# Optimization experiments

Hardware: AMD Instinct MI355X
Metric: run time of the kernel (lower is better)

Reference implementation:

```python
import jax, jax.numpy as jnp
import numpy as np

B, S, H, NH = 2, 2048, 1024, 16
HD = H // NH  # 64


def rope_cos_sin(seq_len, dim, base=10000.0, dtype=jnp.float32):
    inv_freq = 1.0 / (base ** (jnp.arange(0, dim, 2, dtype=jnp.float32) / dim))
    t = jnp.arange(seq_len, dtype=jnp.float32)
    freqs = jnp.outer(t, inv_freq)              # [S, dim/2]
    emb = jnp.concatenate([freqs, freqs], -1)   # [S, dim]
    # broadcast shape [1, S, 1, dim]
    return jnp.cos(emb)[None, :, None, :].astype(dtype), jnp.sin(emb)[None, :, None, :].astype(dtype)


def rotate_half(x):
    x1, x2 = x[..., : x.shape[-1] // 2], x[..., x.shape[-1] // 2:]
    return jnp.concatenate([-x2, x1], axis=-1)


def setup_inputs() -> dict:
    key = jax.random.key(0)
    ks = jax.random.split(key, 5)
    sc = 1.0 / np.sqrt(H)
    x = jax.random.normal(ks[0], (B, S, H), jnp.float32)
    Wq = jax.random.normal(ks[1], (H, H), jnp.float32) * sc
    Wk = jax.random.normal(ks[2], (H, H), jnp.float32) * sc
    Wv = jax.random.normal(ks[3], (H, H), jnp.float32) * sc
    Wo = jax.random.normal(ks[4], (H, H), jnp.float32) * sc
    z = jnp.zeros((H,), jnp.float32)
    mask = jnp.tril(jnp.ones((S, S), bool))[None, None]  # causal [1,1,S,S]
    return {"x": x, "Wq": Wq, "bq": z, "Wk": Wk, "bk": z, "Wv": Wv, "bv": z,
            "Wo": Wo, "bo": z, "mask": mask}


def reference(x, Wq, bq, Wk, bk, Wv, bv, Wo, bo, mask):
    b, s, _ = x.shape
    q = (x @ Wq.T + bq).reshape(b, s, NH, HD)
    k = (x @ Wk.T + bk).reshape(b, s, NH, HD)
    v = (x @ Wv.T + bv).reshape(b, s, NH, HD)
    cos, sin = rope_cos_sin(s, HD, dtype=x.dtype)
    q = q * cos + rotate_half(q) * sin
    k = k * cos + rotate_half(k) * sin
    # [b, h, s, s] scores, explicit as in original
    scores = jnp.einsum("bqhd,bkhd->bhqk", q, k) / jnp.sqrt(jnp.asarray(HD, x.dtype))
    scores = jnp.where(mask, scores, jnp.asarray(-jnp.inf, x.dtype))
    attn = jax.nn.softmax(scores, axis=-1)
    out = jnp.einsum("bhqk,bkhd->bqhd", attn, v).reshape(b, s, H)
    return out @ Wo.T + bo
```

## Files before the change

### kernel.cpp

```cpp
#include <hip/hip_runtime.h>

typedef __bf16 bf16;
typedef __bf16 bf16x4 __attribute__((ext_vector_type(4)));
typedef __bf16 bf16x8 __attribute__((ext_vector_type(8)));
typedef float floatx4 __attribute__((ext_vector_type(4)));

#define MFMA16(a, b, c) __builtin_amdgcn_mfma_f32_16x16x32_bf16(a, b, c, 0, 0, 0)

__device__ __forceinline__ void load_lds16(const void* g, void* l) {
    __builtin_amdgcn_global_load_lds(
        (const __attribute__((address_space(1))) unsigned int*)g,
        (__attribute__((address_space(3))) unsigned int*)l, 16, 0, 0);
}

__device__ __forceinline__ bf16x8 scale8(bf16x8 a, float s) {
    bf16x8 o;
    #pragma unroll
    for (int i = 0; i < 8; i++) o[i] = (bf16)((float)a[i] * s);
    return o;
}

__global__ __launch_bounds__(256) void cvt_all_kernel(
    const float* __restrict__ x, const float* __restrict__ wq,
    const float* __restrict__ wk, const float* __restrict__ wv,
    const float* __restrict__ wo,
    bf16* __restrict__ xb, bf16* __restrict__ wqb, bf16* __restrict__ wkb,
    bf16* __restrict__ wvb, bf16* __restrict__ wob)
{
    int bid = blockIdx.x;
    const float* src; bf16* dst; int off;
    if (bid < 4096)      { src = x;  dst = xb;  off = bid; }
    else if (bid < 5120) { src = wq; dst = wqb; off = bid - 4096; }
    else if (bid < 6144) { src = wk; dst = wkb; off = bid - 5120; }
    else if (bid < 7168) { src = wv; dst = wvb; off = bid - 6144; }
    else                 { src = wo; dst = wob; off = bid - 7168; }
    int idx = (off * 256 + threadIdx.x) * 4;
    float4 v = *(const float4*)&src[idx];
    bf16x4 o;
    o[0] = (bf16)v.x; o[1] = (bf16)v.y; o[2] = (bf16)v.z; o[3] = (bf16)v.w;
    *(bf16x4*)&dst[idx] = o;
}

__global__ __launch_bounds__(256) void cvt_kernel(const float* __restrict__ x,
                                                  bf16* __restrict__ xb) {
    int idx = (blockIdx.x * 256 + threadIdx.x) * 4;
    float4 v = *(const float4*)&x[idx];
    bf16x4 o;
    o[0] = (bf16)v.x; o[1] = (bf16)v.y; o[2] = (bf16)v.z; o[3] = (bf16)v.w;
    *(bf16x4*)&xb[idx] = o;
}


#define PREP_STAGE()                                                          \
    int u0 = w * 128 + lane;                                                  \
    int u1 = u0 + 64;                                                         \
    int r0_ = u0 >> 2, c0_ = ((u0 & 3) ^ ((r0_ >> 1) & 3)) * 8;               \
    int r1_ = u1 >> 2, c1_ = ((u1 & 3) ^ ((r1_ >> 1) & 3)) * 8;               \
    int du0 = w * 1024;                                                       \
    int du1 = du0 + 512;

#define STAGE_PF(Asrc, Bsrc, arow, brow, sbuf, kk0)                           \
    do {                                                                      \
        load_lds16(&Asrc[(size_t)((arow) + r0_) * 1024 + (kk0) + c0_],        \
                   &As[sbuf][0][0] + du0);                                    \
        load_lds16(&Asrc[(size_t)((arow) + r1_) * 1024 + (kk0) + c1_],        \
                   &As[sbuf][0][0] + du1);                                    \
        load_lds16(&Bsrc[(size_t)((brow) + r0_) * 1024 + (kk0) + c0_],        \
                   &Bs[sbuf][0][0] + du0);                                    \
        load_lds16(&Bsrc[(size_t)((brow) + r1_) * 1024 + (kk0) + c1_],        \
                   &Bs[sbuf][0][0] + du1);                                    \
    } while (0)

#define GEMM_CORE(Asrc, Bsrc, arow, brow)                                     \
    PREP_STAGE()                                                              \
    STAGE_PF(Asrc, Bsrc, arow, brow, 0, 0);                                   \
    _Pragma("unroll 2")                                                       \
    for (int s = 0; s < 32; s++) {                                            \
        int sb = s & 1;                                                       \
        __syncthreads();                                                      \
        if (s + 1 < 32) STAGE_PF(Asrc, Bsrc, arow, brow, sb ^ 1, (s + 1) * 32); \
        bf16x8 af[4], bfr[4];                                                 \
        _Pragma("unroll")                                                     \
        for (int mt = 0; mt < 4; mt++) {                                      \
            int row = wm + mt * 16 + l15;                                     \
            af[mt] = *(const bf16x8*)&As[sb][row][(quad ^ ((row >> 1) & 3)) * 8]; \
        }                                                                     \
        _Pragma("unroll")                                                     \
        for (int nt = 0; nt < 4; nt++) {                                      \
            int row = wn + nt * 16 + l15;                                     \
            bfr[nt] = *(const bf16x8*)&Bs[sb][row][(quad ^ ((row >> 1) & 3)) * 8]; \
        }                                                                     \
        _Pragma("unroll")                                                     \
        for (int mt = 0; mt < 4; mt++)                                        \
            _Pragma("unroll")                                                 \
            for (int nt = 0; nt < 4; nt++)                                    \
                acc[mt][nt] = MFMA16(af[mt], bfr[nt], acc[mt][nt]);           \
    }

__global__ __launch_bounds__(256) void gemm_qkv_fast(
    const bf16* __restrict__ xb,
    const bf16* __restrict__ Wq, const bf16* __restrict__ Wk,
    const bf16* __restrict__ Wv,
    const float* __restrict__ bq, const float* __restrict__ bk,
    const float* __restrict__ bv,
    bf16* __restrict__ q_ws, bf16* __restrict__ k_ws, bf16* __restrict__ vt_ws)
{
    int m0 = blockIdx.x * 128;
    int n0 = blockIdx.y * 128;
    int sec = n0 >> 10;
    int nw0 = n0 & 1023;
    const bf16* W     = (sec == 0) ? Wq : (sec == 1) ? Wk : Wv;
    const float* bias = (sec == 0) ? bq : (sec == 1) ? bk : bv;

    __shared__ bf16 As[2][128][32];
    __shared__ bf16 Bs[2][128][32];

    int tid = threadIdx.x;
    int lane = tid & 63, w = tid >> 6;
    int l15 = lane & 15, quad = lane >> 4;
    int wm = (w >> 1) * 64, wn = (w & 1) * 64;

    floatx4 acc[4][4];
    #pragma unroll
    for (int i = 0; i < 4; i++)
        #pragma unroll
        for (int j = 0; j < 4; j++) acc[i][j] = (floatx4){0.f, 0.f, 0.f, 0.f};

    GEMM_CORE(xb, W, m0, nw0)

    if (sec < 2) {
        bf16* outp = (sec == 0) ? q_ws : k_ws;
        float inv[2];
        inv[0] = __expf(-(float)l15 * (9.210340371976184f / 32.0f));
        inv[1] = __expf(-(float)(16 + l15) * (9.210340371976184f / 32.0f));
        #pragma unroll
        for (int mt = 0; mt < 4; mt++) {
            #pragma unroll
            for (int r = 0; r < 4; r++) {
                int m = m0 + wm + mt * 16 + quad * 4 + r;
                int bb = m >> 11, s = m & 2047;
                #pragma unroll
                for (int nt = 0; nt < 2; nt++) {
                    int nl1 = nw0 + wn + nt * 16 + l15;
                    int nl2 = nl1 + 32;
                    float x1 = acc[mt][nt][r] + bias[nl1];
                    float x2 = acc[mt][nt + 2][r] + bias[nl2];
                    float ang = (float)s * inv[nt];
                    float sn, cs;
                    __sincosf(ang, &sn, &cs);
                    int hh = nl1 >> 6, d = nl1 & 63;
                    size_t base = ((size_t)(bb * 16 + hh) * 2048 + s) * 64;
                    outp[base + d]      = (bf16)(x1 * cs - x2 * sn);
                    outp[base + d + 32] = (bf16)(x2 * cs + x1 * sn);
                }
            }
        }
    } else {
        #pragma unroll
        for (int mt = 0; mt < 4; mt++) {
            int mbase = m0 + wm + mt * 16 + quad * 4;
            int bb = mbase >> 11, s0 = mbase & 2047;
            #pragma unroll
            for (int nt = 0; nt < 4; nt++) {
                int nl = nw0 + wn + nt * 16 + l15;
                int hh = nl >> 6, d = nl & 63;
                bf16x4 pk;
                #pragma unroll
                for (int r = 0; r < 4; r++) pk[r] = (bf16)(acc[mt][nt][r] + bias[nl]);
                *(bf16x4*)&vt_ws[((size_t)(bb * 16 + hh) * 64 + d) * 2048 + s0] = pk;
            }
        }
    }
}

__global__ __launch_bounds__(256) void gemm_out_fast(
    const bf16* __restrict__ A, const bf16* __restrict__ W,
    const float* __restrict__ bias, float* __restrict__ out)
{
    int m0 = blockIdx.x * 128;
    int n0 = blockIdx.y * 128;

    __shared__ bf16 As[2][128][32];
    __shared__ bf16 Bs[2][128][32];

    int tid = threadIdx.x;
    int lane = tid & 63, w = tid >> 6;
    int l15 = lane & 15, quad = lane >> 4;
    int wm = (w >> 1) * 64, wn = (w & 1) * 64;

    floatx4 acc[4][4];
    #pragma unroll
    for (int i = 0; i < 4; i++)
        #pragma unroll
        for (int j = 0; j < 4; j++) acc[i][j] = (floatx4){0.f, 0.f, 0.f, 0.f};

    GEMM_CORE(A, W, m0, n0)

    #pragma unroll
    for (int mt = 0; mt < 4; mt++) {
        #pragma unroll
        for (int r = 0; r < 4; r++) {
            int m = m0 + wm + mt * 16 + quad * 4 + r;
            #pragma unroll
            for (int nt = 0; nt < 4; nt++) {
                int nl = n0 + wn + nt * 16 + l15;
                out[(size_t)m * 1024 + nl] = acc[mt][nt][r] + bias[nl];
            }
        }
    }
}

__global__ __launch_bounds__(256) void gemm_qkv_f32w(
    const bf16* __restrict__ xb,
    const float* __restrict__ Wq, const float* __restrict__ Wk,
    const float* __restrict__ Wv,
    const float* __restrict__ bq, const float* __restrict__ bk,
    const float* __restrict__ bv,
    bf16* __restrict__ q_ws, bf16* __restrict__ k_ws, bf16* __restrict__ vt_ws)
{
    int m0 = blockIdx.x * 128;
    int n0 = blockIdx.y * 128;
    int sec = n0 >> 10;
    int nw0 = n0 & 1023;
    const float* W    = (sec == 0) ? Wq : (sec == 1) ? Wk : Wv;
    const float* bias = (sec == 0) ? bq : (sec == 1) ? bk : bv;

    __shared__ bf16 As[128][72];
    __shared__ bf16 Bs[128][72];

    int tid = threadIdx.x;
    int lane = tid & 63, w = tid >> 6;
    int l15 = lane & 15, quad = lane >> 4;
    int wm = (w >> 1) * 64, wn = (w & 1) * 64;
    int sr = tid >> 1;
    int sk = (tid & 1) * 32;

    floatx4 acc[4][4];
    #pragma unroll
    for (int i = 0; i < 4; i++)
        #pragma unroll
        for (int j = 0; j < 4; j++) acc[i][j] = (floatx4){0.f, 0.f, 0.f, 0.f};

    for (int k0 = 0; k0 < 1024; k0 += 64) {
        __syncthreads();
        const bf16* ap = &xb[(size_t)(m0 + sr) * 1024 + k0 + sk];
        bf16x8 a0 = *(const bf16x8*)(ap);
        bf16x8 a1 = *(const bf16x8*)(ap + 8);
        bf16x8 a2 = *(const bf16x8*)(ap + 16);
        bf16x8 a3 = *(const bf16x8*)(ap + 24);
        const float* wp = &W[(size_t)(nw0 + sr) * 1024 + k0 + sk];
        bf16x8 bv_[4];
        #pragma unroll
        for (int c = 0; c < 4; c++) {
            float4 f0 = *(const float4*)(wp + c * 8);
            float4 f1 = *(const float4*)(wp + c * 8 + 4);
            bf16x8 t;
            t[0] = (bf16)f0.x; t[1] = (bf16)f0.y; t[2] = (bf16)f0.z; t[3] = (bf16)f0.w;
            t[4] = (bf16)f1.x; t[5] = (bf16)f1.y; t[6] = (bf16)f1.z; t[7] = (bf16)f1.w;
            bv_[c] = t;
        }
        *(bf16x8*)&As[sr][sk + 0]  = a0;
        *(bf16x8*)&As[sr][sk + 8]  = a1;
        *(bf16x8*)&As[sr][sk + 16] = a2;
        *(bf16x8*)&As[sr][sk + 24] = a3;
        #pragma unroll
        for (int c = 0; c < 4; c++) *(bf16x8*)&Bs[sr][sk + c * 8] = bv_[c];
        __syncthreads();
        #pragma unroll
        for (int kk = 0; kk < 64; kk += 32) {
            bf16x8 af[4], bfr[4];
            #pragma unroll
            for (int mt = 0; mt < 4; mt++)
                af[mt] = *(const bf16x8*)&As[wm + mt * 16 + l15][kk + quad * 8];
            #pragma unroll
            for (int nt = 0; nt < 4; nt++)
                bfr[nt] = *(const bf16x8*)&Bs[wn + nt * 16 + l15][kk + quad * 8];
            #pragma unroll
            for (int mt = 0; mt < 4; mt++)
                #pragma unroll
                for (int nt = 0; nt < 4; nt++)
                    acc[mt][nt] = MFMA16(af[mt], bfr[nt], acc[mt][nt]);
        }
    }

    if (sec < 2) {
        bf16* outp = (sec == 0) ? q_ws : k_ws;
        float inv[2];
        inv[0] = __expf(-(float)l15 * (9.210340371976184f / 32.0f));
        inv[1] = __expf(-(float)(16 + l15) * (9.210340371976184f / 32.0f));
        #pragma unroll
        for (int mt = 0; mt < 4; mt++) {
            #pragma unroll
            for (int r = 0; r < 4; r++) {
                int m = m0 + wm + mt * 16 + quad * 4 + r;
                int bb = m >> 11, s = m & 2047;
                #pragma unroll
                for (int nt = 0; nt < 2; nt++) {
                    int nl1 = nw0 + wn + nt * 16 + l15;
                    int nl2 = nl1 + 32;
                    float x1 = acc[mt][nt][r] + bias[nl1];
                    float x2 = acc[mt][nt + 2][r] + bias[nl2];
                    float ang = (float)s * inv[nt];
                    float sn, cs;
                    __sincosf(ang, &sn, &cs);
                    int hh = nl1 >> 6, d = nl1 & 63;
                    size_t base = ((size_t)(bb * 16 + hh) * 2048 + s) * 64;
                    outp[base + d]      = (bf16)(x1 * cs - x2 * sn);
                    outp[base + d + 32] = (bf16)(x2 * cs + x1 * sn);
                }
            }
        }
    } else {
        #pragma unroll
        for (int mt = 0; mt < 4; mt++) {
            int mbase = m0 + wm + mt * 16 + quad * 4;
            int bb = mbase >> 11, s0 = mbase & 2047;
            #pragma unroll
            for (int nt = 0; nt < 4; nt++) {
                int nl = nw0 + wn + nt * 16 + l15;
                int hh = nl >> 6, d = nl & 63;
                bf16x4 pk;
                #pragma unroll
                for (int r = 0; r < 4; r++) pk[r] = (bf16)(acc[mt][nt][r] + bias[nl]);
                *(bf16x4*)&vt_ws[((size_t)(bb * 16 + hh) * 64 + d) * 2048 + s0] = pk;
            }
        }
    }
}

__global__ __launch_bounds__(256) void gemm_out_f32w(
    const bf16* __restrict__ A, const float* __restrict__ W,
    const float* __restrict__ bias, float* __restrict__ out)
{
    int m0 = blockIdx.x * 128;
    int n0 = blockIdx.y * 128;

    __shared__ bf16 As[128][72];
    __shared__ bf16 Bs[128][72];

    int tid = threadIdx.x;
    int lane = tid & 63, w = tid >> 6;
    int l15 = lane & 15, quad = lane >> 4;
    int wm = (w >> 1) * 64, wn = (w & 1) * 64;
    int sr = tid >> 1;
    int sk = (tid & 1) * 32;

    floatx4 acc[4][4];
    #pragma unroll
    for (int i = 0; i < 4; i++)
        #pragma unroll
        for (int j = 0; j < 4; j++) acc[i][j] = (floatx4){0.f, 0.f, 0.f, 0.f};

    for (int k0 = 0; k0 < 1024; k0 += 64) {
        __syncthreads();
        const bf16* ap = &A[(size_t)(m0 + sr) * 1024 + k0 + sk];
        bf16x8 a0 = *(const bf16x8*)(ap);
        bf16x8 a1 = *(const bf16x8*)(ap + 8);
        bf16x8 a2 = *(const bf16x8*)(ap + 16);
        bf16x8 a3 = *(const bf16x8*)(ap + 24);
        const float* wp = &W[(size_t)(n0 + sr) * 1024 + k0 + sk];
        bf16x8 bv_[4];
        #pragma unroll
        for (int c = 0; c < 4; c++) {
            float4 f0 = *(const float4*)(wp + c * 8);
            float4 f1 = *(const float4*)(wp + c * 8 + 4);
            bf16x8 t;
            t[0] = (bf16)f0.x; t[1] = (bf16)f0.y; t[2] = (bf16)f0.z; t[3] = (bf16)f0.w;
            t[4] = (bf16)f1.x; t[5] = (bf16)f1.y; t[6] = (bf16)f1.z; t[7] = (bf16)f1.w;
            bv_[c] = t;
        }
        *(bf16x8*)&As[sr][sk + 0]  = a0;
        *(bf16x8*)&As[sr][sk + 8]  = a1;
        *(bf16x8*)&As[sr][sk + 16] = a2;
        *(bf16x8*)&As[sr][sk + 24] = a3;
        #pragma unroll
        for (int c = 0; c < 4; c++) *(bf16x8*)&Bs[sr][sk + c * 8] = bv_[c];
        __syncthreads();
        #pragma unroll
        for (int kk = 0; kk < 64; kk += 32) {
            bf16x8 af[4], bfr[4];
            #pragma unroll
            for (int mt = 0; mt < 4; mt++)
                af[mt] = *(const bf16x8*)&As[wm + mt * 16 + l15][kk + quad * 8];
            #pragma unroll
            for (int nt = 0; nt < 4; nt++)
                bfr[nt] = *(const bf16x8*)&Bs[wn + nt * 16 + l15][kk + quad * 8];
            #pragma unroll
            for (int mt = 0; mt < 4; mt++)
                #pragma unroll
                for (int nt = 0; nt < 4; nt++)
                    acc[mt][nt] = MFMA16(af[mt], bfr[nt], acc[mt][nt]);
        }
    }

    #pragma unroll
    for (int mt = 0; mt < 4; mt++) {
        #pragma unroll
        for (int r = 0; r < 4; r++) {
            int m = m0 + wm + mt * 16 + quad * 4 + r;
            #pragma unroll
            for (int nt = 0; nt < 4; nt++) {
                int nl = n0 + wn + nt * 16 + l15;
                out[(size_t)m * 1024 + nl] = acc[mt][nt][r] + bias[nl];
            }
        }
    }
}

__global__ __launch_bounds__(512, 4) void attn_kernel(
    const bf16* __restrict__ q_ws, const bf16* __restrict__ k_ws,
    const bf16* __restrict__ vt_ws, bf16* __restrict__ o_ws)
{
    __shared__ bf16 Ks[2][64][64];
    __shared__ bf16 Vt[2][64][64];
    __shared__ bf16 Ps[8][16][72];

    int tid = threadIdx.x;
    int w = tid >> 6, lane = tid & 63;
    int l15 = lane & 15, quad = lane >> 4;

    int bid = blockIdx.x;
    int g = bid & 31;
    int xx = bid >> 5;
    int qt = (xx < 8) ? xx : 23 - xx;
    if (g & 1) qt = 15 - qt;
    int bb = g >> 4, h = g & 15;
    const bf16* qp = q_ws + (size_t)g * 2048 * 64;
    const bf16* kp = k_ws + (size_t)g * 2048 * 64;
    const bf16* vp = vt_ws + (size_t)g * 64 * 2048;
    int qrow = qt * 128 + w * 16;

    int r = w * 8 + (lane >> 3);
    int c = (lane & 7) ^ (r & 7);
    int od = w * 512;

    const float SCL = 0.125f * 1.4426950408889634f;
    const float MFIX = 20.0f;

    bf16x8 qf0 = scale8(*(const bf16x8*)&qp[(size_t)(qrow + l15) * 64 + quad * 8], SCL);
    bf16x8 qf1 = scale8(*(const bf16x8*)&qp[(size_t)(qrow + l15) * 64 + 32 + quad * 8], SCL);

    float l_lane = 0.f;
    floatx4 acc[4];
    #pragma unroll
    for (int nt = 0; nt < 4; nt++) acc[nt] = (floatx4){0.f, 0.f, 0.f, 0.f};

    int nkt = 2 * qt + 2;

    load_lds16(&kp[(size_t)r * 64 + c * 8], &Ks[0][0][0] + od);
    load_lds16(&vp[(size_t)r * 2048 + c * 8], &Vt[0][0][0] + od);

    for (int kt = 0; kt < nkt; kt++) {
        int buf = kt & 1;
        __syncthreads();

        if (kt + 1 < nkt) {
            int kn0 = (kt + 1) * 64;
            load_lds16(&kp[(size_t)(kn0 + r) * 64 + c * 8], &Ks[buf ^ 1][0][0] + od);
            load_lds16(&vp[(size_t)r * 2048 + kn0 + c * 8], &Vt[buf ^ 1][0][0] + od);
        }

        int kt0 = kt * 64;

        floatx4 st[4];
        #pragma unroll
        for (int kb = 0; kb < 4; kb++) {
            int row = kb * 16 + l15;
            int rx = row & 7;
            bf16x8 a0 = *(const bf16x8*)&Ks[buf][row][(quad ^ rx) * 8];
            bf16x8 a1 = *(const bf16x8*)&Ks[buf][row][((quad + 4) ^ rx) * 8];
            floatx4 z = {-MFIX, -MFIX, -MFIX, -MFIX};
            z = MFMA16(a0, qf0, z);
            z = MFMA16(a1, qf1, z);
            st[kb] = z;
        }
        if (kt0 + 63 > qrow) {
            int q = qrow + l15;
            #pragma unroll
            for (int kb = 0; kb < 4; kb++)
                #pragma unroll
                for (int rr = 0; rr < 4; rr++) {
                    int key = kt0 + kb * 16 + quad * 4 + rr;
                    if (key > q) st[kb][rr] = -1e30f;
                }
        }

        #pragma unroll
        for (int kb = 0; kb < 4; kb++) {
            bf16x4 pk;
            #pragma unroll
            for (int rr = 0; rr < 4; rr++) {
                float pv = exp2f(st[kb][rr]);
                l_lane += pv;
                pk[rr] = (bf16)pv;
            }
            *(bf16x4*)&Ps[w][l15][kb * 16 + quad * 4] = pk;
        }

        bf16x8 pb0 = *(const bf16x8*)&Ps[w][l15][quad * 8];
        bf16x8 pb1 = *(const bf16x8*)&Ps[w][l15][32 + quad * 8];
        #pragma unroll
        for (int nt = 0; nt < 4; nt++) {
            int row = nt * 16 + l15;
            int rx = row & 7;
            bf16x8 v0 = *(const bf16x8*)&Vt[buf][row][(quad ^ rx) * 8];
            bf16x8 v1 = *(const bf16x8*)&Vt[buf][row][((quad + 4) ^ rx) * 8];
            acc[nt] = MFMA16(v0, pb0, acc[nt]);
            acc[nt] = MFMA16(v1, pb1, acc[nt]);
        }
    }

    l_lane += __shfl_xor(l_lane, 16, 64);
    l_lane += __shfl_xor(l_lane, 32, 64);
    float inv = 1.f / l_lane;
    int s = qrow + l15;
    #pragma unroll
    for (int nt = 0; nt < 4; nt++) {
        bf16x4 pk;
        #pragma unroll
        for (int rr = 0; rr < 4; rr++) pk[rr] = (bf16)(acc[nt][rr] * inv);
        *(bf16x4*)&o_ws[((size_t)(bb * 2048 + s)) * 1024 + h * 64 + nt * 16 + quad * 4] = pk;
    }
}

extern "C" void kernel_launch(void* const* d_in, const int* in_sizes, int n_in,
                              void* d_out, int out_size, void* d_ws, size_t ws_size,
                              hipStream_t stream) {
    const float* x  = (const float*)d_in[0];
    const float* Wq = (const float*)d_in[1];
    const float* bq = (const float*)d_in[2];
    const float* Wk = (const float*)d_in[3];
    const float* bk = (const float*)d_in[4];
    const float* Wv = (const float*)d_in[5];
    const float* bv = (const float*)d_in[6];
    const float* Wo = (const float*)d_in[7];
    const float* bo = (const float*)d_in[8];
    float* out = (float*)d_out;

    const size_t NELEM = (size_t)2 * 2048 * 1024;
    const size_t WELEM = (size_t)1024 * 1024;
    bf16* xb    = (bf16*)d_ws;
    bf16* q_ws  = xb + NELEM;
    bf16* k_ws  = q_ws + NELEM;
    bf16* vt_ws = k_ws + NELEM;
    bf16* o_ws  = xb;
    bf16* wqb   = vt_ws + NELEM;
    bf16* wkb   = wqb + WELEM;
    bf16* wvb   = wkb + WELEM;
    bf16* wob   = wvb + WELEM;

    bool fast = ws_size >= (size_t)40 * 1024 * 1024;

    if (fast) {
        cvt_all_kernel<<<8192, 256, 0, stream>>>(x, Wq, Wk, Wv, Wo,
                                                 xb, wqb, wkb, wvb, wob);
        gemm_qkv_fast<<<dim3(32, 24), 256, 0, stream>>>(
            xb, wqb, wkb, wvb, bq, bk, bv, q_ws, k_ws, vt_ws);
        attn_kernel<<<512, 512, 0, stream>>>(q_ws, k_ws, vt_ws, o_ws);
        gemm_out_fast<<<dim3(32, 8), 256, 0, stream>>>(o_ws, wob, bo, out);
    } else {
        cvt_kernel<<<4096, 256, 0, stream>>>(x, xb);
        gemm_qkv_f32w<<<dim3(32, 24), 256, 0, stream>>>(
            xb, Wq, Wk, Wv, bq, bk, bv, q_ws, k_ws, vt_ws);
        attn_kernel<<<512, 512, 0, stream>>>(q_ws, k_ws, vt_ws, o_ws);
        gemm_out_f32w<<<dim3(32, 8), 256, 0, stream>>>(o_ws, Wo, bo, out);
    }
}
```

Baseline: 215.2 us.

## Use explicit vmcnt waits and split barriers with MFMA priority in GEMM and attention

Replaces the __syncthreads at the top of each K-loop iteration with a sequence that issues the next stage's global-to-LDS prefetch first. It then waits only on the previous stage's loads via s_waitcnt vmcnt(N) before barriering, and adds a trailing lgkmcnt barrier at the end of each iteration. The MFMA blocks are wrapped in s_setprio(1) so compute waves get issue priority over memory-issuing waves. The aim is to keep the next tile's loads in flight while the current tile is computed. The vmcnt counts are hand-tuned to the number of loads issued per thread, so any change to the load count would silently break correctness.

```diff
diff --git a/kernel.cpp b/kernel.cpp
--- a/kernel.cpp
+++ b/kernel.cpp
@@ -19,6 +19,19 @@
     for (int i = 0; i < 8; i++) o[i] = (bf16)((float)a[i] * s);
     return o;
 }
+
+#define WAITV4_BAR()  do { asm volatile("s_waitcnt vmcnt(4)" ::: "memory"); \
+                           __builtin_amdgcn_s_barrier();                    \
+                           __builtin_amdgcn_sched_barrier(0); } while (0)
+#define WAITV2_BAR()  do { asm volatile("s_waitcnt vmcnt(2)" ::: "memory"); \
+                           __builtin_amdgcn_s_barrier();                    \
+                           __builtin_amdgcn_sched_barrier(0); } while (0)
+#define WAITV0_BAR()  do { asm volatile("s_waitcnt vmcnt(0)" ::: "memory"); \
+                           __builtin_amdgcn_s_barrier();                    \
+                           __builtin_amdgcn_sched_barrier(0); } while (0)
+#define TRAIL_BAR()   do { __builtin_amdgcn_sched_barrier(0);               \
+                           asm volatile("s_waitcnt lgkmcnt(0)" ::: "memory"); \
+                           __builtin_amdgcn_s_barrier(); } while (0)
 
 __global__ __launch_bounds__(256) void cvt_all_kernel(
     const float* __restrict__ x, const float* __restrict__ wq,
@@ -77,8 +90,12 @@
     _Pragma("unroll 2")                                                       \
     for (int s = 0; s < 32; s++) {                                            \
         int sb = s & 1;                                                       \
-        __syncthreads();                                                      \
-        if (s + 1 < 32) STAGE_PF(Asrc, Bsrc, arow, brow, sb ^ 1, (s + 1) * 32); \
+        if (s + 1 < 32) {                                                     \
+            STAGE_PF(Asrc, Bsrc, arow, brow, sb ^ 1, (s + 1) * 32);           \
+            WAITV4_BAR();                                                     \
+        } else {                                                              \
+            WAITV0_BAR();                                                     \
+        }                                                                     \
         bf16x8 af[4], bfr[4];                                                 \
         _Pragma("unroll")                                                     \
         for (int mt = 0; mt < 4; mt++) {                                      \
@@ -90,11 +107,14 @@
             int row = wn + nt * 16 + l15;                                     \
             bfr[nt] = *(const bf16x8*)&Bs[sb][row][(quad ^ ((row >> 1) & 3)) * 8]; \
         }                                                                     \
+        __builtin_amdgcn_s_setprio(1);                                        \
         _Pragma("unroll")                                                     \
         for (int mt = 0; mt < 4; mt++)                                        \
             _Pragma("unroll")                                                 \
             for (int nt = 0; nt < 4; nt++)                                    \
                 acc[mt][nt] = MFMA16(af[mt], bfr[nt], acc[mt][nt]);           \
+        __builtin_amdgcn_s_setprio(0);                                        \
+        TRAIL_BAR();                                                          \
     }
 
 __global__ __launch_bounds__(256) void gemm_qkv_fast(
@@ -452,12 +472,13 @@
 
     for (int kt = 0; kt < nkt; kt++) {
         int buf = kt & 1;
-        __syncthreads();
-
         if (kt + 1 < nkt) {
             int kn0 = (kt + 1) * 64;
             load_lds16(&kp[(size_t)(kn0 + r) * 64 + c * 8], &Ks[buf ^ 1][0][0] + od);
             load_lds16(&vp[(size_t)r * 2048 + kn0 + c * 8], &Vt[buf ^ 1][0][0] + od);
+            WAITV2_BAR();
+        } else {
+            WAITV0_BAR();
         }
 
         int kt0 = kt * 64;
@@ -470,8 +491,10 @@
             bf16x8 a0 = *(const bf16x8*)&Ks[buf][row][(quad ^ rx) * 8];
             bf16x8 a1 = *(const bf16x8*)&Ks[buf][row][((quad + 4) ^ rx) * 8];
             floatx4 z = {-MFIX, -MFIX, -MFIX, -MFIX};
+            __builtin_amdgcn_s_setprio(1);
             z = MFMA16(a0, qf0, z);
             z = MFMA16(a1, qf1, z);
+            __builtin_amdgcn_s_setprio(0);
             st[kb] = z;
         }
         if (kt0 + 63 > qrow) {
@@ -499,6 +522,7 @@
 
         bf16x8 pb0 = *(const bf16x8*)&Ps[w][l15][quad * 8];
         bf16x8 pb1 = *(const bf16x8*)&Ps[w][l15][32 + quad * 8];
+        __builtin_amdgcn_s_setprio(1);
         #pragma unroll
         for (int nt = 0; nt < 4; nt++) {
             int row = nt * 16 + l15;
@@ -508,6 +532,9 @@
             acc[nt] = MFMA16(v0, pb0, acc[nt]);
             acc[nt] = MFMA16(v1, pb1, acc[nt]);
         }
+        __builtin_amdgcn_s_setprio(0);
+
+        TRAIL_BAR();
     }
 
     l_lane += __shfl_xor(l_lane, 16, 64);
```

Measured after the change: 202.6 us. -5.8%, faster.
